# Kernel optimization log

Hardware: AMD Instinct MI355X
Metric: run time of the kernel (lower is better)

The kernel has to match this reference:

```python
import jax, jax.numpy as jnp
import numpy as np

B, T, D, H, W = 2, 8192, 512, 8, 256
d = D // H  # 64
NC = T // W  # number of chunks (T divisible by W)


def setup_inputs() -> dict:
    key = jax.random.key(0)
    ks = jax.random.split(key, 9)
    s = 1.0 / np.sqrt(D).astype(np.float32)
    x = jax.random.normal(ks[0], (B, T, D), jnp.float32)
    Wq = jax.random.normal(ks[1], (D, D), jnp.float32) * s
    Wk = jax.random.normal(ks[2], (D, D), jnp.float32) * s
    Wv = jax.random.normal(ks[3], (D, D), jnp.float32) * s
    Wo = jax.random.normal(ks[4], (D, D), jnp.float32) * s
    bq = jax.random.normal(ks[5], (D,), jnp.float32) * 0.01
    bk = jax.random.normal(ks[6], (D,), jnp.float32) * 0.01
    bv = jax.random.normal(ks[7], (D,), jnp.float32) * 0.01
    bo = jax.random.normal(ks[8], (D,), jnp.float32) * 0.01
    return {"x": x, "Wq": Wq, "bq": bq, "Wk": Wk, "bk": bk,
            "Wv": Wv, "bv": bv, "Wo": Wo, "bo": bo}


def _local_attention(q, k, v):
    # q, k, v: [B, H, T, d]. Each W-sized query chunk attends to keys in
    # [chunk_start - W, chunk_end + W) -> a 3W window, masked at boundaries.
    qc = q.reshape(B, H, NC, W, d)
    pad = ((0, 0), (0, 0), (W, W), (0, 0))
    kp = jnp.pad(k, pad)
    vp = jnp.pad(v, pad)
    # window gather indices into padded sequence: [NC, 3W]
    pos = jnp.arange(NC)[:, None] * W + jnp.arange(3 * W)[None, :]
    kw = kp[:, :, pos, :]  # [B, H, NC, 3W, d]
    vw = vp[:, :, pos, :]  # [B, H, NC, 3W, d]
    valid = (pos >= W) & (pos < T + W)  # [NC, 3W] true for real (unpadded) keys
    scores = jnp.einsum('bhcqd,bhckd->bhcqk', qc, kw) * (d ** -0.5)
    scores = jnp.where(valid[None, None, :, None, :], scores, -jnp.inf)
    attn = jax.nn.softmax(scores, axis=-1)
    out = jnp.einsum('bhcqk,bhckd->bhcqd', attn, vw)
    return out.reshape(B, H, T, d)


def reference(x, Wq, bq, Wk, bk, Wv, bv, Wo, bo):
    # Linear = x @ W.T + b (torch nn.Linear convention)
    q = (x @ Wq.T + bq).reshape(B, T, H, d).transpose(0, 2, 1, 3)
    # k_proj / v_proj run under torch.no_grad() in the original
    k = jax.lax.stop_gradient(x @ Wk.T + bk).reshape(B, T, H, d).transpose(0, 2, 1, 3)
    v = jax.lax.stop_gradient(x @ Wv.T + bv).reshape(B, T, H, d).transpose(0, 2, 1, 3)
    out = _local_attention(q, k, v)           # [B, H, T, d]
    out = out.transpose(0, 2, 1, 3).reshape(B, T, D)
    return out @ Wo.T + bo
```

## Files before the change

### kernel.cpp

```cpp
#include <hip/hip_runtime.h>
#include <hip/hip_bf16.h>

typedef unsigned short u16;
typedef unsigned int   u32;
typedef __bf16 bf16x8 __attribute__((ext_vector_type(8)));
typedef float  f32x4  __attribute__((ext_vector_type(4)));

#define BB 2
#define TT 8192
#define DD 512
#define HH 8
#define WW 256
#define DH 64
#define NX 8388608
#define NW 262144

__device__ __forceinline__ float b2f(u16 u) {
    unsigned int x = ((unsigned int)u) << 16;
    return __builtin_bit_cast(float, x);
}
__device__ __forceinline__ u16 f2b(float f) {
    __bf16 h = (__bf16)f;
    return __builtin_bit_cast(u16, h);
}
__device__ __forceinline__ bf16x8 ldsfrag(const u16* p) {
    return *(const bf16x8*)p;
}
__device__ __forceinline__ f32x4 mfma16(bf16x8 a, bf16x8 b, f32x4 c) {
    return __builtin_amdgcn_mfma_f32_16x16x32_bf16(a, b, c, 0, 0, 0);
}

typedef __attribute__((address_space(1))) u32 gu32;
typedef __attribute__((address_space(3))) u32 lu32;
__device__ __forceinline__ void gl_lds(const u16* g, u16* l) {
    __builtin_amdgcn_global_load_lds((gu32*)g, (lu32*)l, 16, 0, 0);
}

__device__ __forceinline__ void cvt8(const void* s, u16* d, long i, int f) {
    if (f) {
        const u32* sp = (const u32*)s + i;
        uint4 a = *(const uint4*)(sp);
        uint4 b = *(const uint4*)(sp + 4);
        u16 o[8];
        o[0] = f2b(__builtin_bit_cast(float, a.x));
        o[1] = f2b(__builtin_bit_cast(float, a.y));
        o[2] = f2b(__builtin_bit_cast(float, a.z));
        o[3] = f2b(__builtin_bit_cast(float, a.w));
        o[4] = f2b(__builtin_bit_cast(float, b.x));
        o[5] = f2b(__builtin_bit_cast(float, b.y));
        o[6] = f2b(__builtin_bit_cast(float, b.z));
        o[7] = f2b(__builtin_bit_cast(float, b.w));
        *(uint4*)(d + i) = *(const uint4*)o;
    } else {
        *(uint4*)(d + i) = *(const uint4*)((const u16*)s + i);
    }
}

__global__ void convert_all(const void* x, const void* Wq, const void* bq,
                            const void* Wk, const void* bk, const void* Wv,
                            const void* bv, const void* Wo, const void* bo,
                            u16* __restrict__ xb, u16* __restrict__ Wcat,
                            u16* __restrict__ Wob, u16* __restrict__ bcat,
                            u16* __restrict__ bob, int* __restrict__ flagw)
{
    __shared__ int sflag;
    const int tid = threadIdx.x;
    if (tid == 0) sflag = 0;
    __syncthreads();
    int mybad = 0;
    for (int i = tid; i < 2048; i += 256) {
        float v = b2f(((const u16*)x)[i]);
        if (!(fabsf(v) < 100.f)) mybad = 1;
    }
    if (mybad) atomicOr(&sflag, 1);
    __syncthreads();
    const int f = sflag ? 1 : 0;
    if (blockIdx.x == 0 && tid == 0) *flagw = f;

    long i = ((long)blockIdx.x * 256 + tid) * 8;
    if (i < NX)            { cvt8(x,  xb,           i, f); return; }
    i -= NX;
    if (i < NW)            { cvt8(Wq, Wcat,         i, f); return; }
    i -= NW;
    if (i < NW)            { cvt8(Wk, Wcat + NW,    i, f); return; }
    i -= NW;
    if (i < NW)            { cvt8(Wv, Wcat + 2*NW,  i, f); return; }
    i -= NW;
    if (i < NW)            { cvt8(Wo, Wob,          i, f); return; }
    i -= NW;
    if (i < 512)           { cvt8(bq, bcat,         i, f); return; }
    i -= 512;
    if (i < 512)           { cvt8(bk, bcat + 512,   i, f); return; }
    i -= 512;
    if (i < 512)           { cvt8(bv, bcat + 1024,  i, f); return; }
    i -= 512;
    if (i < 512)           { cvt8(bo, bob,          i, f); }
}

__global__ __launch_bounds__(256, 2)
void gemm128(const u16* __restrict__ A, const u16* __restrict__ Bw,
             const u16* __restrict__ bias, void* __restrict__ out0,
             u16* __restrict__ out1, u16* __restrict__ out2,
             int mode, const int* __restrict__ flagp)
{
    __shared__ __align__(16) u16 AsF[128 * 64];
    __shared__ __align__(16) u16 BsF[128 * 64];

    const int tid  = threadIdx.x;
    const int lane = tid & 63;
    const int wv   = tid >> 6;
    const int col  = lane & 15;
    const int quad = lane >> 4;
    const int wm   = (wv & 1) * 64;
    const int wn   = (wv >> 1) * 64;
    const int m0   = blockIdx.x * 128;
    const int n0   = blockIdx.y * 128;

    f32x4 acc[4][4] = {};

    for (int k0 = 0; k0 < 512; k0 += 64) {
        __syncthreads();
        #pragma unroll
        for (int i = 0; i < 4; i++) {
            const int r  = (wv * 4 + i) * 8 + (lane >> 3);
            const int cb = (lane & 7) ^ (r & 7);
            gl_lds(A  + (size_t)(m0 + r) * 512 + k0 + cb * 8, &AsF[(wv * 4 + i) * 512]);
            gl_lds(Bw + (size_t)(n0 + r) * 512 + k0 + cb * 8, &BsF[(wv * 4 + i) * 512]);
        }
        __syncthreads();
        #pragma unroll
        for (int kk = 0; kk < 2; kk++) {
            bf16x8 fa[4], fb[4];
            #pragma unroll
            for (int mi = 0; mi < 4; mi++)
                fa[mi] = ldsfrag(&AsF[(wm + mi * 16 + col) * 64 + ((kk * 4 + quad) ^ (col & 7)) * 8]);
            #pragma unroll
            for (int ni = 0; ni < 4; ni++)
                fb[ni] = ldsfrag(&BsF[(wn + ni * 16 + col) * 64 + ((kk * 4 + quad) ^ (col & 7)) * 8]);
            #pragma unroll
            for (int mi = 0; mi < 4; mi++)
                #pragma unroll
                for (int ni = 0; ni < 4; ni++)
                    acc[mi][ni] = mfma16(fa[mi], fb[ni], acc[mi][ni]);
        }
    }

    if (mode == 0) {
        #pragma unroll
        for (int ni = 0; ni < 4; ni++) {
            const int gn = n0 + wn + ni * 16 + col;
            const float bv = b2f(bias[gn]);
            const int seg = gn >> 9;
            #pragma unroll
            for (int mi = 0; mi < 4; mi++) {
                const int gmb = m0 + wm + mi * 16 + quad * 4;
                if (seg < 2) {
                    u16* dst = (seg == 0) ? (u16*)out0 : out1;
                    #pragma unroll
                    for (int r = 0; r < 4; r++)
                        dst[(size_t)(gmb + r) * 512 + (gn & 511)] = f2b(acc[mi][ni][r] + bv);
                } else {
                    const int d = gn & 63, hh = (gn >> 6) & 7;
                    const int bb = gmb >> 13, t = gmb & 8191;
                    u16 pb[4];
                    #pragma unroll
                    for (int r = 0; r < 4; r++) pb[r] = f2b(acc[mi][ni][r] + bv);
                    uint2 pk;
                    pk.x = pb[0] | ((u32)pb[1] << 16);
                    pk.y = pb[2] | ((u32)pb[3] << 16);
                    *(uint2*)&out2[((size_t)(bb * 8 + hh) * 64 + d) * 8192 + t] = pk;
                }
            }
        }
    } else {
        const int outf32 = *flagp;
        #pragma unroll
        for (int ni = 0; ni < 4; ni++) {
            const int gn = n0 + wn + ni * 16 + col;
            const float bv = b2f(bias[gn]);
            #pragma unroll
            for (int mi = 0; mi < 4; mi++) {
                #pragma unroll
                for (int r = 0; r < 4; r++) {
                    const int gm = m0 + wm + mi * 16 + quad * 4 + r;
                    const float v = acc[mi][ni][r] + bv;
                    if (outf32) ((float*)out0)[(size_t)gm * 512 + gn] = v;
                    else        ((u16*)out0)[(size_t)gm * 512 + gn]  = f2b(v);
                }
            }
        }
    }
}

#define PSW 72
__global__ __launch_bounds__(512, 4)
void attn_local(const u16* __restrict__ Qg, const u16* __restrict__ Kg,
                const u16* __restrict__ VTg, u16* __restrict__ Og)
{
    __shared__ __align__(16) u16 Ks[2][64 * 64];
    __shared__ __align__(16) u16 VTs[2][64 * 64];
    __shared__ __align__(16) u16 Ps[8][32 * PSW];

    const int tid  = threadIdx.x;
    const int lane = tid & 63;
    const int wv   = tid >> 6;
    const int col  = lane & 15;
    const int quad = lane >> 4;

    const int idx = blockIdx.x;
    const int c = idx & 31;
    const int h = (idx >> 5) & 7;
    const int b = idx >> 8;

    const int t0 = c * WW;
    const int wq = wv * 32;

    const int sc_lo = (c == 0) ? 4 : 0;
    const int nsc   = (c == 0 || c == 31) ? 8 : 12;

    const int ldr = lane >> 3;
    const int ldc = lane & 7;

    bf16x8 qf[2][2];
    {
        const size_t qbase = ((size_t)(b * TT + t0 + wq + col)) * DD + h * DH + quad * 8;
        #pragma unroll
        for (int qi = 0; qi < 2; qi++)
            #pragma unroll
            for (int kk = 0; kk < 2; kk++)
                qf[qi][kk] = *(const bf16x8*)(Qg + qbase + (size_t)qi * 16 * DD + kk * 32);
    }

    f32x4 o[4][2] = {};
    float lsum[2] = {0.f, 0.f};

    u16* psb = &Ps[wv][0];

    {
        const int kstart = t0 - WW + sc_lo * 64;
        const int rr = wv * 8 + ldr;
        const int cb = ldc ^ (rr & 7);
        gl_lds(Kg  + ((size_t)(b * TT + kstart + rr)) * DD + h * DH + cb * 8,
               &Ks[0][wv * 512]);
        gl_lds(VTg + ((size_t)((b * HH + h) * DH + rr)) * TT + kstart + cb * 8,
               &VTs[0][wv * 512]);
    }

    for (int it = 0; it < nsc; it++) {
        __syncthreads();
        if (it + 1 < nsc) {
            const int kstart = t0 - WW + (sc_lo + it + 1) * 64;
            const int buf = (it + 1) & 1;
            const int rr = wv * 8 + ldr;
            const int cb = ldc ^ (rr & 7);
            gl_lds(Kg  + ((size_t)(b * TT + kstart + rr)) * DD + h * DH + cb * 8,
                   &Ks[buf][wv * 512]);
            gl_lds(VTg + ((size_t)((b * HH + h) * DH + rr)) * TT + kstart + cb * 8,
                   &VTs[buf][wv * 512]);
        }
        const u16* ks = &Ks[it & 1][0];
        const u16* vs = &VTs[it & 1][0];

        f32x4 s[4][2];
        #pragma unroll
        for (int ns = 0; ns < 4; ns++)
            #pragma unroll
            for (int qi = 0; qi < 2; qi++)
                s[ns][qi] = (f32x4){0.f, 0.f, 0.f, 0.f};
        #pragma unroll
        for (int ns = 0; ns < 4; ns++) {
            const int row = ns * 16 + col;
            bf16x8 ka0 = ldsfrag(&ks[row * 64 + ((0 + quad) ^ (col & 7)) * 8]);
            bf16x8 ka1 = ldsfrag(&ks[row * 64 + ((4 + quad) ^ (col & 7)) * 8]);
            #pragma unroll
            for (int qi = 0; qi < 2; qi++) {
                s[ns][qi] = mfma16(ka0, qf[qi][0], s[ns][qi]);
                s[ns][qi] = mfma16(ka1, qf[qi][1], s[ns][qi]);
            }
        }

        #pragma unroll
        for (int ns = 0; ns < 4; ns++) {
            #pragma unroll
            for (int qi = 0; qi < 2; qi++) {
                u16 pb[4];
                #pragma unroll
                for (int r = 0; r < 4; r++) {
                    const float p = __expf(s[ns][qi][r] * 0.125f);
                    pb[r] = f2b(p);
                    lsum[qi] += p;
                }
                uint2 pk;
                pk.x = pb[0] | ((u32)pb[1] << 16);
                pk.y = pb[2] | ((u32)pb[3] << 16);
                *(uint2*)&psb[(qi * 16 + col) * PSW + ns * 16 + quad * 4] = pk;
            }
        }
        asm volatile("" ::: "memory");

        #pragma unroll
        for (int kt = 0; kt < 2; kt++) {
            bf16x8 pf[2];
            #pragma unroll
            for (int qi = 0; qi < 2; qi++)
                pf[qi] = ldsfrag(&psb[(qi * 16 + col) * PSW + kt * 32 + quad * 8]);
            #pragma unroll
            for (int di = 0; di < 4; di++) {
                bf16x8 va = ldsfrag(&vs[(di * 16 + col) * 64 + ((kt * 4 + quad) ^ (col & 7)) * 8]);
                #pragma unroll
                for (int qi = 0; qi < 2; qi++)
                    o[di][qi] = mfma16(va, pf[qi], o[di][qi]);
            }
        }
    }

    #pragma unroll
    for (int qi = 0; qi < 2; qi++) {
        float l = lsum[qi];
        l += __shfl_xor(l, 16);
        l += __shfl_xor(l, 32);
        lsum[qi] = 1.0f / l;
    }

    #pragma unroll
    for (int qi = 0; qi < 2; qi++) {
        const size_t ob = ((size_t)(b * TT + t0 + wq + qi * 16 + col)) * DD + h * DH + quad * 4;
        #pragma unroll
        for (int di = 0; di < 4; di++) {
            u16 pb[4];
            #pragma unroll
            for (int r = 0; r < 4; r++) pb[r] = f2b(o[di][qi][r] * lsum[qi]);
            uint2 pk;
            pk.x = pb[0] | ((u32)pb[1] << 16);
            pk.y = pb[2] | ((u32)pb[3] << 16);
            *(uint2*)&Og[ob + di * 16] = pk;
        }
    }
}

extern "C" void kernel_launch(void* const* d_in, const int* in_sizes, int n_in,
                              void* d_out, int out_size, void* d_ws, size_t ws_size,
                              hipStream_t stream)
{
    u16* ws   = (u16*)d_ws;
    u16* xb   = ws;
    u16* Wcat = xb + NX;
    u16* Wob  = Wcat + 3 * NW;
    u16* bcat = Wob + NW;
    u16* bob  = bcat + 1536;
    u16* qws  = bob + 512;
    u16* kws  = qws + NX;
    u16* vtws = kws + NX;
    u16* aws  = vtws + NX;
    int* flag = (int*)(aws + NX);

    convert_all<<<4609, 256, 0, stream>>>(
        d_in[0], d_in[1], d_in[2], d_in[3], d_in[4], d_in[5], d_in[6], d_in[7], d_in[8],
        xb, Wcat, Wob, bcat, bob, flag);

    gemm128<<<dim3(128, 12), 256, 0, stream>>>(xb, Wcat, bcat, qws, kws, vtws, 0, flag);
    attn_local<<<dim3(BB * HH * 32), 512, 0, stream>>>(qws, kws, vtws, aws);
    gemm128<<<dim3(128, 4), 256, 0, stream>>>(aws, Wob, bob, d_out, nullptr, nullptr, 1, flag);
}
```

Measured before the change: 195.7 us.

## Triple-buffer GEMM LDS stages with async prefetch and split waitcnt barriers

Replaces the single-buffer 64-wide K loop in the projection GEMM with a three-stage ring of 32-wide K tiles. Each tile is prefetched two steps ahead, with explicit vmcnt waits and raw barriers so global-to-LDS loads overlap MFMA work. The goal is to hide load latency that the previous sync-load-sync pattern exposed. In exchange there are more barriers per K (16 steps instead of 8), a new swizzle, and launch bounds raised to 3 blocks per CU, which may pressure registers.

```diff
diff --git a/kernel.cpp b/kernel.cpp
--- a/kernel.cpp
+++ b/kernel.cpp
@@ -97,14 +97,14 @@
     if (i < 512)           { cvt8(bo, bob,          i, f); }
 }
 
-__global__ __launch_bounds__(256, 2)
+__global__ __launch_bounds__(256, 3)
 void gemm128(const u16* __restrict__ A, const u16* __restrict__ Bw,
              const u16* __restrict__ bias, void* __restrict__ out0,
              u16* __restrict__ out1, u16* __restrict__ out2,
              int mode, const int* __restrict__ flagp)
 {
-    __shared__ __align__(16) u16 AsF[128 * 64];
-    __shared__ __align__(16) u16 BsF[128 * 64];
+    __shared__ __align__(16) u16 AsF[3][128 * 32];
+    __shared__ __align__(16) u16 BsF[3][128 * 32];
 
     const int tid  = threadIdx.x;
     const int lane = tid & 63;
@@ -118,31 +118,79 @@
 
     f32x4 acc[4][4] = {};
 
-    for (int k0 = 0; k0 < 512; k0 += 64) {
-        __syncthreads();
-        #pragma unroll
-        for (int i = 0; i < 4; i++) {
-            const int r  = (wv * 4 + i) * 8 + (lane >> 3);
-            const int cb = (lane & 7) ^ (r & 7);
-            gl_lds(A  + (size_t)(m0 + r) * 512 + k0 + cb * 8, &AsF[(wv * 4 + i) * 512]);
-            gl_lds(Bw + (size_t)(n0 + r) * 512 + k0 + cb * 8, &BsF[(wv * 4 + i) * 512]);
-        }
-        __syncthreads();
-        #pragma unroll
-        for (int kk = 0; kk < 2; kk++) {
-            bf16x8 fa[4], fb[4];
-            #pragma unroll
-            for (int mi = 0; mi < 4; mi++)
-                fa[mi] = ldsfrag(&AsF[(wm + mi * 16 + col) * 64 + ((kk * 4 + quad) ^ (col & 7)) * 8]);
+    const int srow = lane >> 2;
+    const int scol = lane & 3;
+
+    auto STAGE = [&](int buf, int k0) {
+        #pragma unroll
+        for (int i = 0; i < 2; i++) {
+            const int r  = wv * 32 + i * 16 + srow;
+            const int cb = scol ^ (r & 3);
+            gl_lds(A  + (size_t)(m0 + r) * 512 + k0 + cb * 8, &AsF[buf][(wv * 2 + i) * 512]);
+            gl_lds(Bw + (size_t)(n0 + r) * 512 + k0 + cb * 8, &BsF[buf][(wv * 2 + i) * 512]);
+        }
+    };
+
+    const int rdo = (quad ^ (col & 3)) * 8;
+
+    STAGE(0, 0);
+    STAGE(1, 32);
+    asm volatile("s_waitcnt vmcnt(4) lgkmcnt(0)" ::: "memory");
+    __builtin_amdgcn_s_barrier();
+    __builtin_amdgcn_sched_barrier(0);
+
+    int cur = 0;
+    for (int t = 0; t < 14; t++) {
+        const int stg = (cur == 0) ? 2 : cur - 1;
+        STAGE(stg, (t + 2) * 32);
+        bf16x8 fa[4], fb[4];
+        #pragma unroll
+        for (int mi = 0; mi < 4; mi++)
+            fa[mi] = ldsfrag(&AsF[cur][(wm + mi * 16 + col) * 32 + rdo]);
+        #pragma unroll
+        for (int ni = 0; ni < 4; ni++)
+            fb[ni] = ldsfrag(&BsF[cur][(wn + ni * 16 + col) * 32 + rdo]);
+        #pragma unroll
+        for (int mi = 0; mi < 4; mi++)
             #pragma unroll
             for (int ni = 0; ni < 4; ni++)
-                fb[ni] = ldsfrag(&BsF[(wn + ni * 16 + col) * 64 + ((kk * 4 + quad) ^ (col & 7)) * 8]);
-            #pragma unroll
-            for (int mi = 0; mi < 4; mi++)
-                #pragma unroll
-                for (int ni = 0; ni < 4; ni++)
-                    acc[mi][ni] = mfma16(fa[mi], fb[ni], acc[mi][ni]);
-        }
+                acc[mi][ni] = mfma16(fa[mi], fb[ni], acc[mi][ni]);
+        asm volatile("s_waitcnt vmcnt(4) lgkmcnt(0)" ::: "memory");
+        __builtin_amdgcn_s_barrier();
+        __builtin_amdgcn_sched_barrier(0);
+        cur = (cur == 2) ? 0 : cur + 1;
+    }
+    {
+        bf16x8 fa[4], fb[4];
+        #pragma unroll
+        for (int mi = 0; mi < 4; mi++)
+            fa[mi] = ldsfrag(&AsF[cur][(wm + mi * 16 + col) * 32 + rdo]);
+        #pragma unroll
+        for (int ni = 0; ni < 4; ni++)
+            fb[ni] = ldsfrag(&BsF[cur][(wn + ni * 16 + col) * 32 + rdo]);
+        #pragma unroll
+        for (int mi = 0; mi < 4; mi++)
+            #pragma unroll
+            for (int ni = 0; ni < 4; ni++)
+                acc[mi][ni] = mfma16(fa[mi], fb[ni], acc[mi][ni]);
+        asm volatile("s_waitcnt vmcnt(0) lgkmcnt(0)" ::: "memory");
+        __builtin_amdgcn_s_barrier();
+        __builtin_amdgcn_sched_barrier(0);
+        cur = (cur == 2) ? 0 : cur + 1;
+    }
+    {
+        bf16x8 fa[4], fb[4];
+        #pragma unroll
+        for (int mi = 0; mi < 4; mi++)
+            fa[mi] = ldsfrag(&AsF[cur][(wm + mi * 16 + col) * 32 + rdo]);
+        #pragma unroll
+        for (int ni = 0; ni < 4; ni++)
+            fb[ni] = ldsfrag(&BsF[cur][(wn + ni * 16 + col) * 32 + rdo]);
+        #pragma unroll
+        for (int mi = 0; mi < 4; mi++)
+            #pragma unroll
+            for (int ni = 0; ni < 4; ni++)
+                acc[mi][ni] = mfma16(fa[mi], fb[ni], acc[mi][ni]);
     }
 
     if (mode == 0) {
```

New measurement: 204.7 us. +4.6%, slower.

## Use 256x128 GEMM tiles with triple-buffered async LDS prefetch pipeline

Applied to the files above, without the earlier changes.

Replaces the 128x128 GEMM kernel with a 256x128 tile, 512-thread version that triple-buffers A/B tiles in LDS. Global-to-LDS loads for step k+2 are issued in the middle of the MFMA phases, with explicit vmcnt waits, barriers and setprio, so memory latency overlaps compute. The intent is to remove the per-k-step load/sync stalls of the single-buffered loop. In exchange it uses more LDS (about 144KB per block) and launches fewer blocks, which may limit occupancy. The hand-placed wait counts are fragile.

```diff
diff --git a/kernel.cpp b/kernel.cpp
--- a/kernel.cpp
+++ b/kernel.cpp
@@ -97,52 +97,82 @@
     if (i < 512)           { cvt8(bo, bob,          i, f); }
 }
 
-__global__ __launch_bounds__(256, 2)
-void gemm128(const u16* __restrict__ A, const u16* __restrict__ Bw,
+__global__ __launch_bounds__(512, 2)
+void gemm256(const u16* __restrict__ A, const u16* __restrict__ Bw,
              const u16* __restrict__ bias, void* __restrict__ out0,
              u16* __restrict__ out1, u16* __restrict__ out2,
              int mode, const int* __restrict__ flagp)
 {
-    __shared__ __align__(16) u16 AsF[128 * 64];
-    __shared__ __align__(16) u16 BsF[128 * 64];
+    __shared__ __align__(16) u16 AsF[3][256 * 64];
+    __shared__ __align__(16) u16 BsF[3][128 * 64];
 
     const int tid  = threadIdx.x;
     const int lane = tid & 63;
     const int wv   = tid >> 6;
     const int col  = lane & 15;
     const int quad = lane >> 4;
-    const int wm   = (wv & 1) * 64;
-    const int wn   = (wv >> 1) * 64;
-    const int m0   = blockIdx.x * 128;
+    const int wm   = (wv >> 1) * 64;
+    const int wn   = (wv & 1) * 64;
+    const int m0   = blockIdx.x * 256;
     const int n0   = blockIdx.y * 128;
 
     f32x4 acc[4][4] = {};
 
-    for (int k0 = 0; k0 < 512; k0 += 64) {
-        __syncthreads();
-        #pragma unroll
-        for (int i = 0; i < 4; i++) {
-            const int r  = (wv * 4 + i) * 8 + (lane >> 3);
-            const int cb = (lane & 7) ^ (r & 7);
-            gl_lds(A  + (size_t)(m0 + r) * 512 + k0 + cb * 8, &AsF[(wv * 4 + i) * 512]);
-            gl_lds(Bw + (size_t)(n0 + r) * 512 + k0 + cb * 8, &BsF[(wv * 4 + i) * 512]);
-        }
-        __syncthreads();
-        #pragma unroll
-        for (int kk = 0; kk < 2; kk++) {
-            bf16x8 fa[4], fb[4];
-            #pragma unroll
-            for (int mi = 0; mi < 4; mi++)
-                fa[mi] = ldsfrag(&AsF[(wm + mi * 16 + col) * 64 + ((kk * 4 + quad) ^ (col & 7)) * 8]);
+    const int lr  = lane >> 3;
+    const int lc  = lane & 7;
+    const int cbs = lc ^ lr;
+
+    auto STG = [&](int buf, int k0, int half) {
+        #pragma unroll
+        for (int i = 0; i < 2; i++) {
+            const int g = wv * 4 + half * 2 + i;
+            gl_lds(A + (size_t)(m0 + g * 8 + lr) * 512 + k0 + cbs * 8,
+                   &AsF[buf][g * 512]);
+        }
+        const int g2 = wv * 2 + half;
+        gl_lds(Bw + (size_t)(n0 + g2 * 8 + lr) * 512 + k0 + cbs * 8,
+               &BsF[buf][g2 * 512]);
+    };
+
+    auto PHASE = [&](int p, int kk, int q, int k2, int half, int dostage, int endw) {
+        bf16x8 fa[4], fb[4];
+        #pragma unroll
+        for (int mi = 0; mi < 4; mi++)
+            fa[mi] = ldsfrag(&AsF[p][(wm + mi * 16 + col) * 64 + ((kk * 4 + quad) ^ (col & 7)) * 8]);
+        #pragma unroll
+        for (int ni = 0; ni < 4; ni++)
+            fb[ni] = ldsfrag(&BsF[p][(wn + ni * 16 + col) * 64 + ((kk * 4 + quad) ^ (col & 7)) * 8]);
+        if (dostage) STG(q, k2, half);
+        __builtin_amdgcn_s_barrier();
+        asm volatile("s_waitcnt lgkmcnt(0)" ::: "memory");
+        __builtin_amdgcn_sched_barrier(0);
+        __builtin_amdgcn_s_setprio(1);
+        #pragma unroll
+        for (int mi = 0; mi < 4; mi++)
             #pragma unroll
             for (int ni = 0; ni < 4; ni++)
-                fb[ni] = ldsfrag(&BsF[(wn + ni * 16 + col) * 64 + ((kk * 4 + quad) ^ (col & 7)) * 8]);
-            #pragma unroll
-            for (int mi = 0; mi < 4; mi++)
-                #pragma unroll
-                for (int ni = 0; ni < 4; ni++)
-                    acc[mi][ni] = mfma16(fa[mi], fb[ni], acc[mi][ni]);
-        }
+                acc[mi][ni] = mfma16(fa[mi], fb[ni], acc[mi][ni]);
+        __builtin_amdgcn_s_setprio(0);
+        if (endw == 6)      asm volatile("s_waitcnt vmcnt(6)" ::: "memory");
+        else if (endw == 0) asm volatile("s_waitcnt vmcnt(0)" ::: "memory");
+        __builtin_amdgcn_s_barrier();
+        __builtin_amdgcn_sched_barrier(0);
+    };
+
+    STG(0, 0, 0);  STG(0, 0, 1);
+    STG(1, 64, 0); STG(1, 64, 1);
+    asm volatile("s_waitcnt vmcnt(6)" ::: "memory");
+    __builtin_amdgcn_s_barrier();
+    __builtin_amdgcn_sched_barrier(0);
+
+    #pragma unroll
+    for (int t = 0; t < 8; t++) {
+        const int p  = t % 3;
+        const int q  = (t + 2) % 3;
+        const int k2 = (t + 2) * 64;
+        const int st = (t < 6) ? 1 : 0;
+        PHASE(p, 0, q, k2, 0, st, -1);
+        PHASE(p, 1, q, k2, 1, st, (t < 6) ? 6 : ((t == 6) ? 0 : -1));
     }
 
     if (mode == 0) {
@@ -358,7 +388,7 @@
         d_in[0], d_in[1], d_in[2], d_in[3], d_in[4], d_in[5], d_in[6], d_in[7], d_in[8],
         xb, Wcat, Wob, bcat, bob, flag);
 
-    gemm128<<<dim3(128, 12), 256, 0, stream>>>(xb, Wcat, bcat, qws, kws, vtws, 0, flag);
+    gemm256<<<dim3(64, 12), 512, 0, stream>>>(xb, Wcat, bcat, qws, kws, vtws, 0, flag);
     attn_local<<<dim3(BB * HH * 32), 512, 0, stream>>>(qws, kws, vtws, aws);
-    gemm128<<<dim3(128, 4), 256, 0, stream>>>(aws, Wob, bob, d_out, nullptr, nullptr, 1, flag);
-}
+    gemm256<<<dim3(64, 4), 512, 0, stream>>>(aws, Wob, bob, d_out, nullptr, nullptr, 1, flag);
+}
```

After: 193.0 us. About the same (-1.4%).
